# Kernel tuning notes

Measured on AMD Instinct MI355X. Metric: run time of the kernel, lower is better.

## Reference

```python
import jax, jax.numpy as jnp
import numpy as np

NUM_EXPERTS = 8
TOP_K = 2


def setup_inputs() -> dict:
    key = jax.random.key(0)
    k1, k2 = jax.random.split(key)
    N, D = 8192, 4096
    inputs = jax.random.normal(k1, (N, D), dtype=jnp.float32)
    # torch.nn.Linear weight is [out_features, in_features] = [E, D]
    gate_w = jax.random.normal(k2, (NUM_EXPERTS, D), dtype=jnp.float32) * (1.0 / np.sqrt(D))
    return {"inputs": inputs, "gate_w": gate_w}


def reference(inputs, gate_w):
    # gate linear (no bias): [N, D] x [D, E] -> [N, E]
    router_logits = jnp.einsum("nd,ed->ne", inputs.astype(jnp.float32), gate_w)
    router_weights = jax.nn.softmax(router_logits, axis=1)
    # top-k over experts, renormalize selected weights
    sel_w, sel_idx = jax.lax.top_k(router_weights, TOP_K)          # [N, K]
    sel_w = sel_w / jnp.sum(sel_w, axis=-1, keepdims=True)
    # dense equivalent of the per-expert torch.where dispatch:
    # combine[n, e] = renormalized weight of token n for expert e (0 if not selected).
    onehot = jax.nn.one_hot(sel_idx, NUM_EXPERTS, dtype=sel_w.dtype)  # [N, K, E]
    combine = jnp.einsum("nk,nke->ne", sel_w, onehot)               # [N, E]
    return combine, sel_idx
```

## Files before the change

kernel.cpp:

```cpp
#include <hip/hip_runtime.h>
#include <math.h>

#define N_TOK 8192
#define DIM   4096
#define NEXP  8
#define TPW   4
#define ITERS (DIM / 256)

__global__ __launch_bounds__(256, 2) void router_kernel(
    const float* __restrict__ x,
    const float* __restrict__ w,
    float* __restrict__ out)
{
    const int lane   = threadIdx.x & 63;
    const int waveid = threadIdx.x >> 6;
    const int group  = blockIdx.x * 4 + waveid;
    const int n0     = group * TPW;

    float acc[TPW][NEXP];
    #pragma unroll
    for (int t = 0; t < TPW; ++t)
        #pragma unroll
        for (int e = 0; e < NEXP; ++e) acc[t][e] = 0.0f;

    const float* xp = x + (size_t)n0 * DIM + lane * 4;
    const float* wp = w + lane * 4;

    float4 xb[4][TPW];
    float4 wb[2][NEXP];

    #pragma unroll
    for (int t = 0; t < TPW; ++t)
        xb[0][t] = *(const float4*)(xp + (size_t)t * DIM);
    #pragma unroll
    for (int e = 0; e < NEXP; ++e)
        wb[0][e] = *(const float4*)(wp + (size_t)e * DIM);
    #pragma unroll
    for (int t = 0; t < TPW; ++t)
        xb[1][t] = *(const float4*)(xp + (size_t)t * DIM + 256);
    #pragma unroll
    for (int t = 0; t < TPW; ++t)
        xb[2][t] = *(const float4*)(xp + (size_t)t * DIM + 512);

    #pragma unroll
    for (int j = 0; j < ITERS; ++j) {
        if (j + 1 < ITERS) {
            const int off = (j + 1) * 256;
            #pragma unroll
            for (int e = 0; e < NEXP; ++e)
                wb[(j + 1) & 1][e] = *(const float4*)(wp + (size_t)e * DIM + off);
        }
        if (j + 3 < ITERS) {
            const int off = (j + 3) * 256;
            #pragma unroll
            for (int t = 0; t < TPW; ++t)
                xb[(j + 3) & 3][t] = *(const float4*)(xp + (size_t)t * DIM + off);
        }

        #pragma unroll
        for (int t = 0; t < TPW; ++t) {
            const float4 xv = xb[j & 3][t];
            #pragma unroll
            for (int e = 0; e < NEXP; ++e) {
                const float4 wv = wb[j & 1][e];
                acc[t][e] = fmaf(xv.x, wv.x,
                            fmaf(xv.y, wv.y,
                            fmaf(xv.z, wv.z,
                            fmaf(xv.w, wv.w, acc[t][e]))));
            }
        }
    }

    #pragma unroll
    for (int t = 0; t < TPW; ++t) {
        #pragma unroll
        for (int e = 0; e < NEXP; ++e) {
            float v = acc[t][e];
            #pragma unroll
            for (int off = 32; off >= 1; off >>= 1)
                v += __shfl_xor(v, off, 64);
            acc[t][e] = v;
        }
    }

    #pragma unroll
    for (int t = 0; t < TPW; ++t) {
        float m1 = acc[t][0]; int i1 = 0;
        #pragma unroll
        for (int e = 1; e < NEXP; ++e)
            if (acc[t][e] > m1) { m1 = acc[t][e]; i1 = e; }
        float m2 = -INFINITY; int i2 = 0;
        #pragma unroll
        for (int e = 0; e < NEXP; ++e)
            if (e != i1 && acc[t][e] > m2) { m2 = acc[t][e]; i2 = e; }

        const float e2  = expf(m2 - m1);
        const float inv = 1.0f / (1.0f + e2);
        const float w1  = inv;
        const float w2  = e2 * inv;

        if (lane == 0) {
            const int n = n0 + t;
            float c[8];
            #pragma unroll
            for (int e = 0; e < 8; ++e)
                c[e] = (e == i1) ? w1 : ((e == i2) ? w2 : 0.0f);
            float4* cp = (float4*)(out + (size_t)n * 8);
            cp[0] = make_float4(c[0], c[1], c[2], c[3]);
            cp[1] = make_float4(c[4], c[5], c[6], c[7]);
            float* ip = out + (size_t)N_TOK * 8 + (size_t)n * 2;
            ip[0] = (float)i1;
            ip[1] = (float)i2;
        }
    }
}

extern "C" void kernel_launch(void* const* d_in, const int* in_sizes, int n_in,
                              void* d_out, int out_size, void* d_ws, size_t ws_size,
                              hipStream_t stream) {
    const float* x = (const float*)d_in[0];
    const float* w = (const float*)d_in[1];
    float* out = (float*)d_out;

    dim3 grid(N_TOK / (4 * TPW));
    dim3 block(256);
    hipLaunchKernelGGL(router_kernel, grid, block, 0, stream, x, w, out);
}
```

Measured before the change: 35.99 us.

## Stage gate weights in shared memory and use 512-thread blocks

Each block first copies the full 8x4096 gate weight matrix (128 KB) into LDS, then the waves read weight fragments from LDS instead of issuing global loads per wave. Blocks grow to 8 waves covering 32 tokens, so the grid shrinks to 256 blocks. The goal is to cut redundant global and L2 traffic for the weights. The cost is a serialized 128 KB preload per block plus a barrier. The large LDS footprint also limits blocks per CU and may leave too few waves to hide x-load latency.

```diff
diff --git a/kernel.cpp b/kernel.cpp
--- a/kernel.cpp
+++ b/kernel.cpp
@@ -5,17 +5,32 @@
 #define DIM   4096
 #define NEXP  8
 #define TPW   4
+#define WAVES 8
+#define TPB   (TPW * WAVES)
+#define NBLK  (N_TOK / TPB)
 #define ITERS (DIM / 256)
 
-__global__ __launch_bounds__(256, 2) void router_kernel(
+__global__ __launch_bounds__(512, 2) void router_kernel(
     const float* __restrict__ x,
     const float* __restrict__ w,
     float* __restrict__ out)
 {
-    const int lane   = threadIdx.x & 63;
-    const int waveid = threadIdx.x >> 6;
-    const int group  = blockIdx.x * 4 + waveid;
-    const int n0     = group * TPW;
+    __shared__ float wl[NEXP][DIM];
+
+    const int tid  = threadIdx.x;
+    const int lane = tid & 63;
+    const int wid  = tid >> 6;
+    const int n0   = blockIdx.x * TPB + wid * TPW;
+
+    #pragma unroll
+    for (int e = 0; e < NEXP; ++e) {
+        #pragma unroll
+        for (int p = 0; p < 2; ++p) {
+            const int pos = p * 2048 + tid * 4;
+            *(float4*)&wl[e][pos] = *(const float4*)(w + (size_t)e * DIM + pos);
+        }
+    }
+    __syncthreads();
 
     float acc[TPW][NEXP];
     #pragma unroll
@@ -24,32 +39,16 @@
         for (int e = 0; e < NEXP; ++e) acc[t][e] = 0.0f;
 
     const float* xp = x + (size_t)n0 * DIM + lane * 4;
-    const float* wp = w + lane * 4;
 
     float4 xb[4][TPW];
-    float4 wb[2][NEXP];
-
     #pragma unroll
-    for (int t = 0; t < TPW; ++t)
-        xb[0][t] = *(const float4*)(xp + (size_t)t * DIM);
-    #pragma unroll
-    for (int e = 0; e < NEXP; ++e)
-        wb[0][e] = *(const float4*)(wp + (size_t)e * DIM);
-    #pragma unroll
-    for (int t = 0; t < TPW; ++t)
-        xb[1][t] = *(const float4*)(xp + (size_t)t * DIM + 256);
-    #pragma unroll
-    for (int t = 0; t < TPW; ++t)
-        xb[2][t] = *(const float4*)(xp + (size_t)t * DIM + 512);
+    for (int s = 0; s < 3; ++s)
+        #pragma unroll
+        for (int t = 0; t < TPW; ++t)
+            xb[s][t] = *(const float4*)(xp + (size_t)t * DIM + s * 256);
 
     #pragma unroll
     for (int j = 0; j < ITERS; ++j) {
-        if (j + 1 < ITERS) {
-            const int off = (j + 1) * 256;
-            #pragma unroll
-            for (int e = 0; e < NEXP; ++e)
-                wb[(j + 1) & 1][e] = *(const float4*)(wp + (size_t)e * DIM + off);
-        }
         if (j + 3 < ITERS) {
             const int off = (j + 3) * 256;
             #pragma unroll
@@ -57,16 +56,20 @@
                 xb[(j + 3) & 3][t] = *(const float4*)(xp + (size_t)t * DIM + off);
         }
 
+        float4 wv[NEXP];
+        #pragma unroll
+        for (int e = 0; e < NEXP; ++e)
+            wv[e] = *(const float4*)&wl[e][j * 256 + lane * 4];
+
         #pragma unroll
         for (int t = 0; t < TPW; ++t) {
             const float4 xv = xb[j & 3][t];
             #pragma unroll
             for (int e = 0; e < NEXP; ++e) {
-                const float4 wv = wb[j & 1][e];
-                acc[t][e] = fmaf(xv.x, wv.x,
-                            fmaf(xv.y, wv.y,
-                            fmaf(xv.z, wv.z,
-                            fmaf(xv.w, wv.w, acc[t][e]))));
+                acc[t][e] = fmaf(xv.x, wv[e].x,
+                            fmaf(xv.y, wv[e].y,
+                            fmaf(xv.z, wv[e].z,
+                            fmaf(xv.w, wv[e].w, acc[t][e]))));
             }
         }
     }
@@ -122,7 +125,5 @@
     const float* w = (const float*)d_in[1];
     float* out = (float*)d_out;
 
-    dim3 grid(N_TOK / (4 * TPW));
-    dim3 block(256);
-    hipLaunchKernelGGL(router_kernel, grid, block, 0, stream, x, w, out);
+    hipLaunchKernelGGL(router_kernel, dim3(NBLK), dim3(512), 0, stream, x, w, out);
 }
```

Result: faster. 34.71 us (-3.6%).
